# Performance work log

Hardware: AMD Instinct MI355X
Metric: run time of the kernel (lower is better)

The kernel has to match this reference:

```python
import jax, jax.numpy as jnp
import numpy as np

HEADS = 16
DIM_HEAD = 64
MAX_REL_POS = 1024   # temporal_length
TEXT_LEN = 77
IMG_SCALE = 1.0      # image_cross_attention_scale


def setup_inputs() -> dict:
    key = jax.random.key(0)
    ks = jax.random.split(key, 12)
    B, N, D = 32, 1024, 1024
    CTX = TEXT_LEN + 256
    s = 0.02
    return {
        "x": jax.random.normal(ks[0], (B, N, D), jnp.float32),
        "context": jax.random.normal(ks[1], (B, CTX, D), jnp.float32),
        "W_q": jax.random.normal(ks[2], (D, D), jnp.float32) * s,
        "W_k": jax.random.normal(ks[3], (D, D), jnp.float32) * s,
        "W_v": jax.random.normal(ks[4], (D, D), jnp.float32) * s,
        "W_k_ip": jax.random.normal(ks[5], (D, D), jnp.float32) * s,
        "W_v_ip": jax.random.normal(ks[6], (D, D), jnp.float32) * s,
        "rel_k": jax.random.normal(ks[7], (2 * MAX_REL_POS + 1, DIM_HEAD), jnp.float32) * s,
        "rel_v": jax.random.normal(ks[8], (2 * MAX_REL_POS + 1, DIM_HEAD), jnp.float32) * s,
        "W_out": jax.random.normal(ks[9], (D, D), jnp.float32) * s,
        "b_out": jnp.zeros((D,), jnp.float32),
        "alpha": jnp.zeros((1,), jnp.float32),
    }


def _split_heads(t):
    # [b, n, h*d] -> [b, h, n, d]
    b, n, _ = t.shape
    return t.reshape(b, n, HEADS, DIM_HEAD).transpose(0, 2, 1, 3)


def _merge_heads(t):
    # [b, h, n, d] -> [b, n, h*d]
    b, h, n, d = t.shape
    return t.transpose(0, 2, 1, 3).reshape(b, n, h * d)


def _rel_embeddings(table, len_q, len_k):
    # gather relative-position embeddings: [len_q, len_k, d]
    dist = jnp.arange(len_k)[None, :] - jnp.arange(len_q)[:, None]
    idx = jnp.clip(dist, -MAX_REL_POS, MAX_REL_POS) + MAX_REL_POS
    return table[idx]


def reference(x, context, W_q, W_k, W_v, W_k_ip, W_v_ip, rel_k, rel_v, W_out, b_out, alpha):
    scale = DIM_HEAD ** -0.5
    ctx_text = context[:, :TEXT_LEN, :]
    ctx_img = context[:, TEXT_LEN:, :]

    q = _split_heads(x @ W_q)          # [b,h,i,d]
    k = _split_heads(ctx_text @ W_k)   # [b,h,j,d]
    v = _split_heads(ctx_text @ W_v)

    sim = jnp.einsum('bhid,bhjd->bhij', q, k) * scale
    len_q, len_k = q.shape[2], k.shape[2]
    k2 = _rel_embeddings(rel_k, len_q, len_k)            # [i,j,d]
    sim = sim + jnp.einsum('bhid,ijd->bhij', q, k2) * scale
    attn = jax.nn.softmax(sim, axis=-1)

    out = jnp.einsum('bhij,bhjd->bhid', attn, v)
    v2 = _rel_embeddings(rel_v, len_q, len_k)            # [i,j,d]
    out = out + jnp.einsum('bhij,ijd->bhid', attn, v2)
    out = _merge_heads(out)                              # [b,i,h*d]

    # second image-context KV stream
    k_ip = _split_heads(ctx_img @ W_k_ip)
    v_ip = _split_heads(ctx_img @ W_v_ip)
    sim_ip = jnp.einsum('bhid,bhjd->bhij', q, k_ip) * scale
    attn_ip = jax.nn.softmax(sim_ip, axis=-1)
    out_ip = _merge_heads(jnp.einsum('bhij,bhjd->bhid', attn_ip, v_ip))

    # learnable-scale bypass: out + scale * out_ip * (tanh(alpha)+1)
    out = out + IMG_SCALE * out_ip * (jnp.tanh(alpha[0]) + 1.0)
    return out @ W_out + b_out
```

## Files before the change

kernel.cpp:

```cpp
#include <hip/hip_runtime.h>
#include <math.h>

typedef __bf16 bf16_t;
typedef __bf16 bf16x2 __attribute__((ext_vector_type(2)));
typedef __bf16 bf16x8 __attribute__((ext_vector_type(8)));
typedef float f32x4 __attribute__((ext_vector_type(4)));

#define BATCH   32
#define SEQ     1024
#define DMODEL  1024
#define NHEADS  16
#define DIMH    64
#define TEXTLEN 77
#define IMGLEN  256
#define CTXLEN  333
#define MAXREL  1024

#define MFMA16(a,b,c) __builtin_amdgcn_mfma_f32_16x16x32_bf16(a, b, c, 0, 0, 0)
#define SCALE_LOG2E 0.1803368809f

__device__ __forceinline__ unsigned pk2(float a, float b) {
  union { bf16x2 v; unsigned u; } t;
  t.v[0] = (bf16_t)a; t.v[1] = (bf16_t)b;
  return t.u;
}

__global__ __launch_bounds__(256) void k_cvt_x(const float* __restrict__ in,
                                               bf16_t* __restrict__ out) {
  size_t idx = ((size_t)blockIdx.x * blockDim.x + threadIdx.x) * 8;
  float4 a = *(const float4*)(in + idx);
  float4 b = *(const float4*)(in + idx + 4);
  bf16x8 o;
  o[0] = (bf16_t)a.x; o[1] = (bf16_t)a.y; o[2] = (bf16_t)a.z; o[3] = (bf16_t)a.w;
  o[4] = (bf16_t)b.x; o[5] = (bf16_t)b.y; o[6] = (bf16_t)b.z; o[7] = (bf16_t)b.w;
  *(bf16x8*)(out + idx) = o;
}

__global__ __launch_bounds__(128) void k_cvt_ctx(const float* __restrict__ ctx,
                                                 bf16_t* __restrict__ ctxT,
                                                 bf16_t* __restrict__ ctxI) {
  int row = blockIdx.x;
  int b = row / CTXLEN, t = row - b * CTXLEN;
  const float* src = ctx + (size_t)row * DMODEL + threadIdx.x * 8;
  bf16_t* dst = (t < TEXTLEN)
      ? ctxT + ((size_t)(b * 80 + t)) * DMODEL + threadIdx.x * 8
      : ctxI + ((size_t)(b * IMGLEN + (t - TEXTLEN))) * DMODEL + threadIdx.x * 8;
  float4 a = *(const float4*)(src);
  float4 c = *(const float4*)(src + 4);
  bf16x8 o;
  o[0] = (bf16_t)a.x; o[1] = (bf16_t)a.y; o[2] = (bf16_t)a.z; o[3] = (bf16_t)a.w;
  o[4] = (bf16_t)c.x; o[5] = (bf16_t)c.y; o[6] = (bf16_t)c.z; o[7] = (bf16_t)c.w;
  *(bf16x8*)dst = o;
  if (t == 0) {
    bf16x8 z = {};
    #pragma unroll
    for (int rr = 77; rr < 80; ++rr)
      *(bf16x8*)(ctxT + ((size_t)(b * 80 + rr)) * DMODEL + threadIdx.x * 8) = z;
  }
}

__global__ void k_transpose_w(const float* __restrict__ W, bf16_t* __restrict__ WT) {
  __shared__ float tile[32][33];
  int x = threadIdx.x, y = threadIdx.y;
  int n0 = blockIdx.x * 32, k0 = blockIdx.y * 32;
  #pragma unroll
  for (int r = 0; r < 32; r += 8)
    tile[y + r][x] = W[(size_t)(k0 + y + r) * DMODEL + n0 + x];
  __syncthreads();
  #pragma unroll
  for (int r = 0; r < 32; r += 8)
    WT[(size_t)(n0 + y + r) * DMODEL + k0 + x] = (bf16_t)tile[x][y + r];
}

__global__ __launch_bounds__(256) void k_cvt_relk(const float* __restrict__ relk,
                                                  bf16_t* __restrict__ Rkb) {
  int idx = blockIdx.x * 256 + threadIdx.x;
  int u = idx >> 3, d0 = (idx & 7) * 8;
  const float* s = relk + (size_t)(u + 1) * DIMH + d0;
  float4 a = *(const float4*)s;
  float4 b = *(const float4*)(s + 4);
  bf16x8 o;
  o[0] = (bf16_t)a.x; o[1] = (bf16_t)a.y; o[2] = (bf16_t)a.z; o[3] = (bf16_t)a.w;
  o[4] = (bf16_t)b.x; o[5] = (bf16_t)b.y; o[6] = (bf16_t)b.z; o[7] = (bf16_t)b.w;
  *(bf16x8*)(Rkb + (size_t)u * DIMH + d0) = o;
}

__global__ __launch_bounds__(256) void k_cvt_relvT(const float* __restrict__ relv,
                                                   bf16_t* __restrict__ RvT) {
  int idx = blockIdx.x * 256 + threadIdx.x;
  int d = idx >> 8, u0 = (idx & 255) * 8;
  bf16x8 o;
  #pragma unroll
  for (int e = 0; e < 8; ++e)
    o[e] = (bf16_t)relv[(size_t)(u0 + e + 1) * DIMH + d];
  *(bf16x8*)(RvT + (size_t)d * 2048 + u0) = o;
}

typedef __attribute__((address_space(1))) void gvoid;
typedef __attribute__((address_space(3))) void svoid;

__device__ __forceinline__ void async_ld16(const void* g, void* l) {
  __builtin_amdgcn_global_load_lds((gvoid*)g, (svoid*)l, 16, 0, 0);
}

template<int STORE, bool AHM>
__global__ __launch_bounds__(512) void k_gemm(
    const bf16_t* __restrict__ A16, const bf16_t* __restrict__ BT,
    void* __restrict__ Cout, void* __restrict__ Cout2,
    const float* __restrict__ bias, int M, int N, int K)
{
  __shared__ __align__(16) bf16_t lds_a[2][256 * 32];
  __shared__ __align__(16) bf16_t lds_b[2][128 * 32];
  const int tid = threadIdx.x;
  const int wid = tid >> 6, lane = tid & 63;
  const int nx = gridDim.x, ny = gridDim.y;
  const int lin = blockIdx.y * nx + blockIdx.x;
  const int nwg = nx * ny;
  const int swz = (lin & 7) * (nwg >> 3) + (lin >> 3);
  const int bcol = (swz % ny) * 128;
  const int brow = (swz / ny) * 256;
  const int wr = (wid >> 1) * 64, wc = (wid & 1) * 64;
  const int lhi = lane >> 4, llo = lane & 15;

  auto stage = [&](int kk, int buf) __attribute__((always_inline)) {
    #pragma unroll
    for (int ch = 0; ch < 2; ++ch) {
      int cid = ch * 512 + tid;
      int row = cid >> 2, ccol = cid & 3;
      int gcol = (ccol ^ (row & 3)) << 3;
      const bf16_t* src;
      if constexpr (AHM) {
        int grow = brow + row;
        src = A16 + (((size_t)((grow >> 10) * 16 + (kk >> 6)) * 1024 + (grow & 1023)) << 6)
              + (kk & 32) + gcol;
      } else {
        src = A16 + (size_t)(brow + row) * K + kk + gcol;
      }
      async_ld16(src, (char*)lds_a[buf] + cid * 16);
    }
    {
      int row = tid >> 2, ccol = tid & 3;
      int gcol = (ccol ^ (row & 3)) << 3;
      async_ld16(BT + (size_t)(bcol + row) * K + kk + gcol,
                 (char*)lds_b[buf] + tid * 16);
    }
  };

  f32x4 acc[4][4];
  #pragma unroll
  for (int m = 0; m < 4; ++m)
    #pragma unroll
    for (int n = 0; n < 4; ++n)
      acc[m][n] = (f32x4){0.f, 0.f, 0.f, 0.f};

  stage(0, 0);
  int cur = 0;
  for (int kk = 0; kk < K; kk += 32) {
    if (kk + 32 < K) {
      stage(kk + 32, cur ^ 1);
      __builtin_amdgcn_sched_barrier(0);
      asm volatile("s_waitcnt vmcnt(3)" ::: "memory");
      __builtin_amdgcn_sched_barrier(0);
    } else {
      asm volatile("s_waitcnt vmcnt(0)" ::: "memory");
    }
    __builtin_amdgcn_s_barrier();

    bf16x8 af[4], bfv[4];
    #pragma unroll
    for (int m = 0; m < 4; ++m) {
      int row = wr + m * 16 + llo;
      af[m] = *(const bf16x8*)((const char*)lds_a[cur] + row * 64
                               + ((lhi ^ (row & 3)) << 4));
    }
    #pragma unroll
    for (int n = 0; n < 4; ++n) {
      int row = wc + n * 16 + llo;
      bfv[n] = *(const bf16x8*)((const char*)lds_b[cur] + row * 64
                                + ((lhi ^ (row & 3)) << 4));
    }
    #pragma unroll
    for (int m = 0; m < 4; ++m)
      #pragma unroll
      for (int n = 0; n < 4; ++n)
        acc[m][n] = MFMA16(af[m], bfv[n], acc[m][n]);

    asm volatile("s_waitcnt lgkmcnt(0)" ::: "memory");
    __builtin_amdgcn_sched_barrier(0);
    __builtin_amdgcn_s_barrier();
    cur ^= 1;
  }

  #pragma unroll
  for (int m = 0; m < 4; ++m)
    #pragma unroll
    for (int n = 0; n < 4; ++n) {
      const int gc = bcol + wc + n * 16 + llo;
      #pragma unroll
      for (int r = 0; r < 4; ++r) {
        const int gr = brow + wr + m * 16 + lhi * 4 + r;
        float v = acc[m][n][r];
        if constexpr (STORE == 2) {
          ((float*)Cout)[(size_t)gr * N + gc] = v + bias[gc];
        } else if constexpr (STORE == 4) {
          int hh2 = gc >> 6;
          ((bf16_t*)Cout)[((((size_t)((gr >> 10) * 16 + hh2)) << 10) + (gr & 1023)) * 64
                          + (gc & 63)] = (bf16_t)v;
        } else if constexpr (STORE == 5) {
          int bb = (gr * 6554) >> 19;
          int jj = gr - bb * 80;
          int hh2 = (gc & 1023) >> 6;
          bf16_t* dst = (gc < 1024) ? (bf16_t*)Cout : (bf16_t*)Cout2;
          dst[(((size_t)(bb * 16 + hh2) * 80 + jj) << 6) + (gc & 63)] = (bf16_t)v;
        } else {
          int bb = gr >> 8, uu = gr & 255;
          int hh2 = (gc & 1023) >> 6;
          bf16_t* dst = (gc < 1024) ? (bf16_t*)Cout : (bf16_t*)Cout2;
          dst[((((size_t)(bb * 16 + hh2)) << 8) + uu) * 64 + (gc & 63)] = (bf16_t)v;
        }
      }
    }
}

template<int RPB, int OUTC>
__global__ __launch_bounds__(256) void k_vtrans(const bf16_t* __restrict__ V,
                                                bf16_t* __restrict__ Vt) {
  __shared__ bf16_t tile[64][72];
  const int nt = (OUTC + 63) / 64;
  const int u0 = (blockIdx.x % nt) * 64;
  const int bh = blockIdx.x / nt;
  const int tid = threadIdx.x;
  const int ur = tid >> 2, cg = (tid & 3) * 16;
  {
    const bf16_t* src = V + (((size_t)bh * RPB + u0 + ur) << 6) + cg;
    *(bf16x8*)&tile[ur][cg] = *(const bf16x8*)src;
    *(bf16x8*)&tile[ur][cg + 8] = *(const bf16x8*)(src + 8);
  }
  __syncthreads();
  bf16x8 o0, o1;
  #pragma unroll
  for (int e = 0; e < 8; ++e) { o0[e] = tile[cg + e][ur]; o1[e] = tile[cg + 8 + e][ur]; }
  bf16_t* dst = Vt + (size_t)bh * 64 * OUTC + (size_t)ur * OUTC + u0 + cg;
  if (u0 + cg + 8 <= OUTC)  *(bf16x8*)dst = o0;
  if (u0 + cg + 16 <= OUTC) *(bf16x8*)(dst + 8) = o1;
}

__global__ __launch_bounds__(256, 2) void k_txt(
    const bf16_t* __restrict__ Qh,
    const bf16_t* __restrict__ Kth,
    const bf16_t* __restrict__ Vtt,
    const bf16_t* __restrict__ Rkb,
    const bf16_t* __restrict__ RvT,
    bf16_t* __restrict__ Oh)
{
  __shared__ __align__(16) bf16_t kt_l[80 * 64];
  __shared__ __align__(16) bf16_t vt_l[64 * 80];
  __shared__ __align__(16) char p_l[4][6400];
  __shared__ __align__(16) char qlds[4][2048];
  __shared__ __align__(16) char olds[4][2048];
  const int tid = threadIdx.x;
  const int w = tid >> 6, lane = tid & 63;
  const int c = lane & 15, g = lane >> 4;
  const int bh = blockIdx.x;

  #pragma unroll
  for (int q = 0; q < 3; ++q) {
    int cid0 = q * 256 + w * 64;
    if (cid0 < 640) {
      int cid = cid0 + lane;
      int row = cid >> 3, cc = cid & 7;
      const bf16_t* src = Kth + (((size_t)bh * 80 + row) << 6) + ((cc ^ (row & 7)) << 3);
      async_ld16(src, (char*)kt_l + cid0 * 16);
    }
  }
  #pragma unroll
  for (int q = 0; q < 3; ++q) {
    int cid0 = q * 256 + w * 64;
    if (cid0 < 640) {
      int cid = cid0 + lane;
      int row = cid / 10;
      int col = cid - row * 10;
      int colp = col - (row & 7); if (colp < 0) colp += 10;
      const bf16_t* src = Vtt + (size_t)bh * 5120 + row * 80 + colp * 8;
      async_ld16(src, (char*)vt_l + cid0 * 16);
    }
  }
  {
    int iq = w * 256;
    #pragma unroll
    for (int k2 = 0; k2 < 2; ++k2) {
      int k = k2 * 64 + lane, rr = k >> 3, cc = k & 7;
      async_ld16(Qh + (((size_t)bh * 1024 + iq + rr) << 6) + ((cc ^ (rr & 7)) << 3),
                 qlds[w] + k2 * 1024);
    }
  }
  __syncthreads();

  bf16_t* p = (bf16_t*)p_l[w];

  for (int st = 0; st < 16; ++st) {
    const int iq = w * 256 + st * 16;
    const int ub = 1008 - iq;
    asm volatile("s_waitcnt vmcnt(0)" ::: "memory");
    bf16x8 qa0 = *(const bf16x8*)(qlds[w] + c * 128 + ((g ^ (c & 7)) << 4));
    bf16x8 qa1 = *(const bf16x8*)(qlds[w] + c * 128 + (((g + 4) ^ (c & 7)) << 4));
    asm volatile("s_waitcnt lgkmcnt(0)" ::: "memory");
    if (st < 15) {
      int iqn = iq + 16;
      #pragma unroll
      for (int k2 = 0; k2 < 2; ++k2) {
        int k = k2 * 64 + lane, rr = k >> 3, cc = k & 7;
        async_ld16(Qh + (((size_t)bh * 1024 + iqn + rr) << 6) + ((cc ^ (rr & 7)) << 3),
                   qlds[w] + k2 * 1024);
      }
    }
    f32x4 ta[6];
    #pragma unroll
    for (int n = 0; n < 6; ++n) ta[n] = (f32x4){0.f, 0.f, 0.f, 0.f};
    {
      const bf16_t* rp = Rkb + (size_t)(ub + c) * DIMH + g * 8;
      #pragma unroll
      for (int n = 0; n < 6; ++n) {
        bf16x8 b0 = *(const bf16x8*)(rp + n * 16 * DIMH);
        bf16x8 b1 = *(const bf16x8*)(rp + n * 16 * DIMH + 32);
        ta[n] = MFMA16(qa0, b0, ta[n]);
        ta[n] = MFMA16(qa1, b1, ta[n]);
      }
    }
    f32x4 s[5];
    #pragma unroll
    for (int n = 0; n < 5; ++n) s[n] = (f32x4){0.f, 0.f, 0.f, 0.f};
    {
      const int sw = (c & 7) << 4;
      #pragma unroll
      for (int n = 0; n < 5; ++n) {
        int rb = (n * 16 + c) * 128;
        bf16x8 k0 = *(const bf16x8*)((const char*)kt_l + rb + ((g << 4) ^ sw));
        bf16x8 k1 = *(const bf16x8*)((const char*)kt_l + rb + (((4 + g) << 4) ^ sw));
        s[n] = MFMA16(qa0, k0, s[n]);
        s[n] = MFMA16(qa1, k1, s[n]);
      }
    }
    float st4[5][4];
    #pragma unroll
    for (int r = 0; r < 4; ++r) {
      int il = 4 * g + r;
      int cz = c + 15 - il;
      int srcl = (lane & 48) | (cz & 15);
      bool lo_pick = (cz >> 4) == 0;
      #pragma unroll
      for (int n = 0; n < 5; ++n) {
        float tlo = __shfl(ta[n][r], srcl);
        float thi = __shfl(ta[n + 1][r], srcl);
        float tv = lo_pick ? tlo : thi;
        int j = 16 * n + c;
        st4[n][r] = (j < TEXTLEN) ? (s[n][r] + tv) : -1e30f;
      }
    }
    float rsum[4];
    #pragma unroll
    for (int r = 0; r < 4; ++r) {
      float m = st4[0][r];
      #pragma unroll
      for (int n = 1; n < 5; ++n) m = fmaxf(m, st4[n][r]);
      m = fmaxf(m, __shfl_xor(m, 1));
      m = fmaxf(m, __shfl_xor(m, 2));
      m = fmaxf(m, __shfl_xor(m, 4));
      m = fmaxf(m, __shfl_xor(m, 8));
      float ssum = 0.f;
      #pragma unroll
      for (int n = 0; n < 5; ++n) {
        float pv = exp2f((st4[n][r] - m) * SCALE_LOG2E);
        st4[n][r] = pv;
        ssum += pv;
      }
      ssum += __shfl_xor(ssum, 1);
      ssum += __shfl_xor(ssum, 2);
      ssum += __shfl_xor(ssum, 4);
      ssum += __shfl_xor(ssum, 8);
      rsum[r] = ssum;
    }
    {
      bf16x8 z8 = {};
      #pragma unroll
      for (int z = 0; z < 7; ++z) {
        int off = z * 1024 + lane * 16;
        if (off < 6400)
          *(bf16x8*)((char*)p + off) = z8;
      }
      #pragma unroll
      for (int n = 0; n < 5; ++n)
        #pragma unroll
        for (int r = 0; r < 4; ++r) {
          int j = 16 * n + c;
          if (j < TEXTLEN) {
            int il = 4 * g + r;
            bf16_t pb = (bf16_t)st4[n][r];
            p[il * 200 + (j + 15 - il)] = pb;
            p[il * 200 + 96 + j] = pb;
          }
        }
    }
    f32x4 ot[4];
    #pragma unroll
    for (int dt = 0; dt < 4; ++dt) ot[dt] = (f32x4){0.f, 0.f, 0.f, 0.f};
    #pragma unroll
    for (int kt = 0; kt < 6; ++kt) {
      bf16x8 pf = *(const bf16x8*)(p + c * 200 + kt * 32 + g * 8);
      int klo = kt * 32 + g * 8;
      #pragma unroll
      for (int dt = 0; dt < 4; ++dt) {
        int d = dt * 16 + c;
        bf16x8 af;
        if (klo < 96) {
          af = *(const bf16x8*)(RvT + (size_t)d * 2048 + ub + klo);
        } else {
          int uv = klo - 96;
          int chunk = (uv >> 3) + (c & 7); if (chunk >= 10) chunk -= 10;
          af = *(const bf16x8*)((const char*)vt_l + d * 160 + chunk * 16);
        }
        ot[dt] = MFMA16(af, pf, ot[dt]);
      }
    }
    int srcq = ((c >> 2) << 4) | c;
    float t0 = __shfl(rsum[0], srcq);
    float t1 = __shfl(rsum[1], srcq);
    float t2 = __shfl(rsum[2], srcq);
    float t3 = __shfl(rsum[3], srcq);
    float rs = (c & 2) ? ((c & 1) ? t3 : t2) : ((c & 1) ? t1 : t0);
    float inv = 1.f / rs;
    #pragma unroll
    for (int dt = 0; dt < 4; ++dt) {
      int chunk = dt * 2 + (g >> 1);
      char* pa = olds[w] + c * 128 + ((chunk ^ (c & 7)) << 4) + (g & 1) * 8;
      uint2 nv;
      nv.x = pk2(ot[dt][0] * inv, ot[dt][1] * inv);
      nv.y = pk2(ot[dt][2] * inv, ot[dt][3] * inv);
      *(uint2*)pa = nv;
    }
    char* ob = (char*)(Oh + (((size_t)bh * 1024 + iq) << 6));
    #pragma unroll
    for (int k2 = 0; k2 < 2; ++k2) {
      int k = k2 * 64 + lane, rr = k >> 3, cc = k & 7;
      uint4 v = *(uint4*)(olds[w] + rr * 128 + ((cc ^ (rr & 7)) << 4));
      *(uint4*)(ob + rr * 128 + cc * 16) = v;
    }
  }
}

__global__ __launch_bounds__(256, 2) void k_img(
    const bf16_t* __restrict__ Qh,
    const bf16_t* __restrict__ Khi,
    const bf16_t* __restrict__ Vipt,
    const float* __restrict__ alpha,
    bf16_t* __restrict__ Oh)
{
  __shared__ __align__(16) bf16_t kst[256 * 64];
  __shared__ __align__(16) bf16_t vst[64 * 256];
  __shared__ __align__(16) char qlds[4][2048];
  __shared__ __align__(16) char olds[4][2048];
  const int tid = threadIdx.x;
  const int w = tid >> 6, lane = tid & 63;
  const int c = lane & 15, g = lane >> 4;
  const int i0 = blockIdx.x * 512;
  const int bh = blockIdx.y;

  #pragma unroll
  for (int q = 0; q < 8; ++q) {
    int cid = q * 256 + tid;
    int row = cid >> 3, cc = cid & 7;
    const bf16_t* src = Khi + (((size_t)bh * 256 + row) << 6) + ((cc ^ (row & 7)) << 3);
    async_ld16(src, (char*)kst + q * 4096 + w * 1024);
  }
  const char* vsrc0 = (const char*)(Vipt + (size_t)bh * 16384);
  #pragma unroll
  for (int q = 0; q < 8; ++q) {
    int L = (q * 256 + tid) * 16;
    int row = L >> 9;
    async_ld16(vsrc0 + (L ^ ((row & 7) << 4)), (char*)vst + q * 4096 + w * 1024);
  }
  {
    int iq = i0 + w * 128;
    #pragma unroll
    for (int k2 = 0; k2 < 2; ++k2) {
      int k = k2 * 64 + lane, rr = k >> 3, cc = k & 7;
      size_t off = (((size_t)bh * 1024 + iq + rr) << 6) + ((cc ^ (rr & 7)) << 3);
      async_ld16(Qh + off, qlds[w] + k2 * 1024);
      async_ld16(Oh + off, olds[w] + k2 * 1024);
    }
  }
  __syncthreads();

  const float coef = tanhf(alpha[0]) + 1.0f;

  for (int st = 0; st < 8; ++st) {
    const int iq = i0 + w * 128 + st * 16;
    asm volatile("s_waitcnt vmcnt(0)" ::: "memory");
    bf16x8 qa0 = *(const bf16x8*)(qlds[w] + c * 128 + ((g ^ (c & 7)) << 4));
    bf16x8 qa1 = *(const bf16x8*)(qlds[w] + c * 128 + (((g + 4) ^ (c & 7)) << 4));
    asm volatile("s_waitcnt lgkmcnt(0)" ::: "memory");
    if (st < 7) {
      int iqn = iq + 16;
      #pragma unroll
      for (int k2 = 0; k2 < 2; ++k2) {
        int k = k2 * 64 + lane, rr = k >> 3, cc = k & 7;
        async_ld16(Qh + (((size_t)bh * 1024 + iqn + rr) << 6) + ((cc ^ (rr & 7)) << 3),
                   qlds[w] + k2 * 1024);
      }
    }
    f32x4 acc[4];
    #pragma unroll
    for (int dt = 0; dt < 4; ++dt) acc[dt] = (f32x4){0.f, 0.f, 0.f, 0.f};
    float m_run = -1e30f, l_run = 0.f;

    #pragma unroll
    for (int jt = 0; jt < 2; ++jt) {
      f32x4 s2[8];
      #pragma unroll
      for (int n = 0; n < 8; ++n) s2[n] = (f32x4){0.f, 0.f, 0.f, 0.f};
      const int sw = (c & 7) << 4;
      #pragma unroll
      for (int n = 0; n < 8; ++n) {
        int rb = (jt * 128 + n * 16 + c) * 128;
        bf16x8 k0 = *(const bf16x8*)((const char*)kst + rb + ((g << 4) ^ sw));
        bf16x8 k1 = *(const bf16x8*)((const char*)kst + rb + (((4 + g) << 4) ^ sw));
        s2[n] = MFMA16(k0, qa0, s2[n]);
        s2[n] = MFMA16(k1, qa1, s2[n]);
      }
      float mx = -1e30f;
      #pragma unroll
      for (int n = 0; n < 8; ++n)
        #pragma unroll
        for (int r = 0; r < 4; ++r) mx = fmaxf(mx, s2[n][r]);
      mx = fmaxf(mx, __shfl_xor(mx, 16));
      mx = fmaxf(mx, __shfl_xor(mx, 32));
      float m_new = fmaxf(m_run, mx);
      float fscale = exp2f((m_run - m_new) * SCALE_LOG2E);
      float tsum = 0.f;
      #pragma unroll
      for (int n = 0; n < 8; ++n)
        #pragma unroll
        for (int r = 0; r < 4; ++r) {
          float pv = exp2f((s2[n][r] - m_new) * SCALE_LOG2E);
          s2[n][r] = pv; tsum += pv;
        }
      tsum += __shfl_xor(tsum, 16);
      tsum += __shfl_xor(tsum, 32);
      l_run = l_run * fscale + tsum;
      m_run = m_new;
      #pragma unroll
      for (int dt = 0; dt < 4; ++dt) acc[dt] *= fscale;
      const int srcA = c | ((g & 1) << 5);
      const int srcB = srcA + 16;
      const bool hi_n = ((g >> 1) & 1) != 0;
      #pragma unroll
      for (int kt = 0; kt < 4; ++kt) {
        unsigned lo0 = pk2(s2[2 * kt][0], s2[2 * kt][1]);
        unsigned hi0 = pk2(s2[2 * kt][2], s2[2 * kt][3]);
        unsigned lo1 = pk2(s2[2 * kt + 1][0], s2[2 * kt + 1][1]);
        unsigned hi1 = pk2(s2[2 * kt + 1][2], s2[2 * kt + 1][3]);
        unsigned a0 = __shfl(lo0, srcA), a1 = __shfl(lo1, srcA);
        unsigned b0 = __shfl(hi0, srcA), b1 = __shfl(hi1, srcA);
        unsigned c0 = __shfl(lo0, srcB), c1 = __shfl(lo1, srcB);
        unsigned d0 = __shfl(hi0, srcB), d1 = __shfl(hi1, srcB);
        union { unsigned u[4]; bf16x8 v; } pf;
        pf.u[0] = hi_n ? a1 : a0;
        pf.u[1] = hi_n ? b1 : b0;
        pf.u[2] = hi_n ? c1 : c0;
        pf.u[3] = hi_n ? d1 : d0;
        #pragma unroll
        for (int dt = 0; dt < 4; ++dt) {
          int d = dt * 16 + c;
          int a = (d * 512 + jt * 256 + kt * 64 + g * 16) ^ ((c & 7) << 4);
          bf16x8 vf = *(const bf16x8*)((const char*)vst + a);
          acc[dt] = MFMA16(vf, pf.v, acc[dt]);
        }
      }
    }
    float inv = coef / l_run;
    asm volatile("s_waitcnt vmcnt(0)" ::: "memory");
    #pragma unroll
    for (int dt = 0; dt < 4; ++dt) {
      int chunk = dt * 2 + (g >> 1);
      char* pa = olds[w] + c * 128 + ((chunk ^ (c & 7)) << 4) + (g & 1) * 8;
      union { uint2 u2; bf16_t e[4]; } ov; ov.u2 = *(uint2*)pa;
      uint2 nv;
      nv.x = pk2((float)ov.e[0] + acc[dt][0] * inv, (float)ov.e[1] + acc[dt][1] * inv);
      nv.y = pk2((float)ov.e[2] + acc[dt][2] * inv, (float)ov.e[3] + acc[dt][3] * inv);
      *(uint2*)pa = nv;
    }
    char* ob = (char*)(Oh + (((size_t)bh * 1024 + iq) << 6));
    #pragma unroll
    for (int k2 = 0; k2 < 2; ++k2) {
      int k = k2 * 64 + lane, rr = k >> 3, cc = k & 7;
      uint4 v = *(uint4*)(olds[w] + rr * 128 + ((cc ^ (rr & 7)) << 4));
      *(uint4*)(ob + rr * 128 + cc * 16) = v;
    }
    asm volatile("s_waitcnt lgkmcnt(0)" ::: "memory");
    if (st < 7) {
      int iqn = iq + 16;
      #pragma unroll
      for (int k2 = 0; k2 < 2; ++k2) {
        int k = k2 * 64 + lane, rr = k >> 3, cc = k & 7;
        async_ld16(Oh + (((size_t)bh * 1024 + iqn + rr) << 6) + ((cc ^ (rr & 7)) << 3),
                   olds[w] + k2 * 1024);
      }
    }
  }
}

extern "C" void kernel_launch(void* const* d_in, const int* in_sizes, int n_in,
                              void* d_out, int out_size, void* d_ws, size_t ws_size,
                              hipStream_t stream)
{
  const float* x     = (const float*)d_in[0];
  const float* ctx   = (const float*)d_in[1];
  const float* W_q   = (const float*)d_in[2];
  const float* W_k   = (const float*)d_in[3];
  const float* W_v   = (const float*)d_in[4];
  const float* W_kip = (const float*)d_in[5];
  const float* W_vip = (const float*)d_in[6];
  const float* rel_k = (const float*)d_in[7];
  const float* rel_v = (const float*)d_in[8];
  const float* W_out = (const float*)d_in[9];
  const float* b_out = (const float*)d_in[10];
  const float* alpha = (const float*)d_in[11];

  char* ws = (char*)d_ws;
  bf16_t* Oh   = (bf16_t*)(ws + 0);
  bf16_t* Qh   = (bf16_t*)(ws + 67108864);
  bf16_t* CtxT = (bf16_t*)(ws + 134217728);
  bf16_t* CtxI = (bf16_t*)(ws + 139460608);
  bf16_t* WTs  = (bf16_t*)(ws + 156237824);
  bf16_t* WqT   = WTs + 0 * 1048576;
  bf16_t* WkT   = WTs + 1 * 1048576;
  bf16_t* WvT   = WTs + 2 * 1048576;
  bf16_t* WkipT = WTs + 3 * 1048576;
  bf16_t* WvipT = WTs + 4 * 1048576;
  bf16_t* WoutT = WTs + 5 * 1048576;

  char* dob = (char*)d_out;
  bf16_t* Khi   = (bf16_t*)(dob + 0);
  bf16_t* Vhi   = (bf16_t*)(dob + 16777216);
  bf16_t* Vipt  = (bf16_t*)(dob + 33554432);
  bf16_t* Kth   = (bf16_t*)(dob + 50331648);
  bf16_t* Vth   = (bf16_t*)(dob + 55574528);
  bf16_t* Vtt   = (bf16_t*)(dob + 60817408);
  bf16_t* Rkb   = (bf16_t*)(dob + 66060288);
  bf16_t* RvT   = (bf16_t*)(dob + 66322432);
  bf16_t* Xb    = (bf16_t*)(dob + 66584576);

  k_cvt_x<<<16384, 256, 0, stream>>>(x, Xb);
  k_cvt_ctx<<<BATCH * CTXLEN, 128, 0, stream>>>(ctx, CtxT, CtxI);
  dim3 tb(32, 8), tg(32, 32);
  k_transpose_w<<<tg, tb, 0, stream>>>(W_q,   WqT);
  k_transpose_w<<<tg, tb, 0, stream>>>(W_k,   WkT);
  k_transpose_w<<<tg, tb, 0, stream>>>(W_v,   WvT);
  k_transpose_w<<<tg, tb, 0, stream>>>(W_kip, WkipT);
  k_transpose_w<<<tg, tb, 0, stream>>>(W_vip, WvipT);
  k_transpose_w<<<tg, tb, 0, stream>>>(W_out, WoutT);
  k_cvt_relk<<<64, 256, 0, stream>>>(rel_k, Rkb);
  k_cvt_relvT<<<64, 256, 0, stream>>>(rel_v, RvT);

  k_gemm<4, false><<<dim3(128, 8),  512, 0, stream>>>(Xb,   WqT,   (void*)Qh,  nullptr,     nullptr, 32768, 1024, 1024);
  k_gemm<5, false><<<dim3(10, 16),  512, 0, stream>>>(CtxT, WkT,   (void*)Kth, (void*)Vth,  nullptr, 2560,  2048, 1024);
  k_gemm<6, false><<<dim3(32, 16),  512, 0, stream>>>(CtxI, WkipT, (void*)Khi, (void*)Vhi,  nullptr, 8192,  2048, 1024);

  k_vtrans<80,  80 ><<<2 * 512, 256, 0, stream>>>(Vth, Vtt);
  k_vtrans<256, 256><<<4 * 512, 256, 0, stream>>>(Vhi, Vipt);

  k_txt<<<512, 256, 0, stream>>>(Qh, Kth, Vtt, Rkb, RvT, Oh);
  k_img<<<dim3(2, 512), 256, 0, stream>>>(Qh, Khi, Vipt, alpha, Oh);

  k_gemm<2, true><<<dim3(128, 8), 512, 0, stream>>>(Oh, WoutT, d_out, nullptr, b_out, 32768, 1024, 1024);
}
```

Measured before the change: 529.5 us.

## Load Q and text V directly from global to cut LDS and raise occupancy

Both attention kernels drop the LDS staging buffer for Q. Instead, each wave loads its Q fragments straight from global memory into registers and prefetches the next tile during the current step. The text kernel also stops staging V^T in LDS and reads it from global, clamping the padded column index. Its launch bound rises to 3 blocks per CU so the freed LDS can buy more occupancy. The trade is more global and L1 traffic inside the inner MFMA loop, plus more register pressure under a tighter bound.

New measurement: 579.8 us. 9.5% more time.

```diff
diff --git a/kernel.cpp b/kernel.cpp
--- a/kernel.cpp
+++ b/kernel.cpp
@@ -245,7 +245,7 @@
   if (u0 + cg + 16 <= OUTC) *(bf16x8*)(dst + 8) = o1;
 }
 
-__global__ __launch_bounds__(256, 2) void k_txt(
+__global__ __launch_bounds__(256, 3) void k_txt(
     const bf16_t* __restrict__ Qh,
     const bf16_t* __restrict__ Kth,
     const bf16_t* __restrict__ Vtt,
@@ -254,9 +254,7 @@
     bf16_t* __restrict__ Oh)
 {
   __shared__ __align__(16) bf16_t kt_l[80 * 64];
-  __shared__ __align__(16) bf16_t vt_l[64 * 80];
   __shared__ __align__(16) char p_l[4][6400];
-  __shared__ __align__(16) char qlds[4][2048];
   __shared__ __align__(16) char olds[4][2048];
   const int tid = threadIdx.x;
   const int w = tid >> 6, lane = tid & 63;
@@ -273,46 +271,27 @@
       async_ld16(src, (char*)kt_l + cid0 * 16);
     }
   }
-  #pragma unroll
-  for (int q = 0; q < 3; ++q) {
-    int cid0 = q * 256 + w * 64;
-    if (cid0 < 640) {
-      int cid = cid0 + lane;
-      int row = cid / 10;
-      int col = cid - row * 10;
-      int colp = col - (row & 7); if (colp < 0) colp += 10;
-      const bf16_t* src = Vtt + (size_t)bh * 5120 + row * 80 + colp * 8;
-      async_ld16(src, (char*)vt_l + cid0 * 16);
-    }
-  }
+  __syncthreads();
+
+  bf16_t* p = (bf16_t*)p_l[w];
+  const bf16_t* qbase = Qh + ((size_t)bh << 16);
+  const bf16_t* vbase = Vtt + (size_t)bh * 5120;
+
+  bf16x8 qa0, qa1;
   {
-    int iq = w * 256;
-    #pragma unroll
-    for (int k2 = 0; k2 < 2; ++k2) {
-      int k = k2 * 64 + lane, rr = k >> 3, cc = k & 7;
-      async_ld16(Qh + (((size_t)bh * 1024 + iq + rr) << 6) + ((cc ^ (rr & 7)) << 3),
-                 qlds[w] + k2 * 1024);
-    }
-  }
-  __syncthreads();
-
-  bf16_t* p = (bf16_t*)p_l[w];
+    const bf16_t* qp = qbase + ((size_t)(w * 256 + c) << 6) + g * 8;
+    qa0 = *(const bf16x8*)qp;
+    qa1 = *(const bf16x8*)(qp + 32);
+  }
 
   for (int st = 0; st < 16; ++st) {
     const int iq = w * 256 + st * 16;
     const int ub = 1008 - iq;
-    asm volatile("s_waitcnt vmcnt(0)" ::: "memory");
-    bf16x8 qa0 = *(const bf16x8*)(qlds[w] + c * 128 + ((g ^ (c & 7)) << 4));
-    bf16x8 qa1 = *(const bf16x8*)(qlds[w] + c * 128 + (((g + 4) ^ (c & 7)) << 4));
-    asm volatile("s_waitcnt lgkmcnt(0)" ::: "memory");
+    bf16x8 qn0 = qa0, qn1 = qa1;
     if (st < 15) {
-      int iqn = iq + 16;
-      #pragma unroll
-      for (int k2 = 0; k2 < 2; ++k2) {
-        int k = k2 * 64 + lane, rr = k >> 3, cc = k & 7;
-        async_ld16(Qh + (((size_t)bh * 1024 + iqn + rr) << 6) + ((cc ^ (rr & 7)) << 3),
-                   qlds[w] + k2 * 1024);
-      }
+      const bf16_t* qp = qbase + ((size_t)(iq + 16 + c) << 6) + g * 8;
+      qn0 = *(const bf16x8*)qp;
+      qn1 = *(const bf16x8*)(qp + 32);
     }
     f32x4 ta[6];
     #pragma unroll
@@ -416,8 +395,8 @@
           af = *(const bf16x8*)(RvT + (size_t)d * 2048 + ub + klo);
         } else {
           int uv = klo - 96;
-          int chunk = (uv >> 3) + (c & 7); if (chunk >= 10) chunk -= 10;
-          af = *(const bf16x8*)((const char*)vt_l + d * 160 + chunk * 16);
+          uv = (uv > 72) ? 72 : uv;
+          af = *(const bf16x8*)(vbase + d * 80 + uv);
         }
         ot[dt] = MFMA16(af, pf, ot[dt]);
       }
@@ -445,6 +424,7 @@
       uint4 v = *(uint4*)(olds[w] + rr * 128 + ((cc ^ (rr & 7)) << 4));
       *(uint4*)(ob + rr * 128 + cc * 16) = v;
     }
+    qa0 = qn0; qa1 = qn1;
   }
 }
 
@@ -457,7 +437,6 @@
 {
   __shared__ __align__(16) bf16_t kst[256 * 64];
   __shared__ __align__(16) bf16_t vst[64 * 256];
-  __shared__ __align__(16) char qlds[4][2048];
   __shared__ __align__(16) char olds[4][2048];
   const int tid = threadIdx.x;
   const int w = tid >> 6, lane = tid & 63;
@@ -484,29 +463,29 @@
     #pragma unroll
     for (int k2 = 0; k2 < 2; ++k2) {
       int k = k2 * 64 + lane, rr = k >> 3, cc = k & 7;
-      size_t off = (((size_t)bh * 1024 + iq + rr) << 6) + ((cc ^ (rr & 7)) << 3);
-      async_ld16(Qh + off, qlds[w] + k2 * 1024);
-      async_ld16(Oh + off, olds[w] + k2 * 1024);
+      async_ld16(Oh + (((size_t)bh * 1024 + iq + rr) << 6) + ((cc ^ (rr & 7)) << 3),
+                 olds[w] + k2 * 1024);
     }
   }
   __syncthreads();
 
   const float coef = tanhf(alpha[0]) + 1.0f;
+  const bf16_t* qbase = Qh + ((size_t)bh << 16);
+
+  bf16x8 qa0, qa1;
+  {
+    const bf16_t* qp = qbase + ((size_t)(i0 + w * 128 + c) << 6) + g * 8;
+    qa0 = *(const bf16x8*)qp;
+    qa1 = *(const bf16x8*)(qp + 32);
+  }
 
   for (int st = 0; st < 8; ++st) {
     const int iq = i0 + w * 128 + st * 16;
-    asm volatile("s_waitcnt vmcnt(0)" ::: "memory");
-    bf16x8 qa0 = *(const bf16x8*)(qlds[w] + c * 128 + ((g ^ (c & 7)) << 4));
-    bf16x8 qa1 = *(const bf16x8*)(qlds[w] + c * 128 + (((g + 4) ^ (c & 7)) << 4));
-    asm volatile("s_waitcnt lgkmcnt(0)" ::: "memory");
+    bf16x8 qn0 = qa0, qn1 = qa1;
     if (st < 7) {
-      int iqn = iq + 16;
-      #pragma unroll
-      for (int k2 = 0; k2 < 2; ++k2) {
-        int k = k2 * 64 + lane, rr = k >> 3, cc = k & 7;
-        async_ld16(Qh + (((size_t)bh * 1024 + iqn + rr) << 6) + ((cc ^ (rr & 7)) << 3),
-                   qlds[w] + k2 * 1024);
-      }
+      const bf16_t* qp = qbase + ((size_t)(iq + 16 + c) << 6) + g * 8;
+      qn0 = *(const bf16x8*)qp;
+      qn1 = *(const bf16x8*)(qp + 32);
     }
     f32x4 acc[4];
     #pragma unroll
@@ -606,6 +585,7 @@
                    olds[w] + k2 * 1024);
       }
     }
+    qa0 = qn0; qa1 = qn1;
   }
 }
 
```
